# Kernel tuning notes

Measured on AMD Instinct MI355X. Metric: run time of the kernel, lower is better.

## Reference

```python
import jax, jax.numpy as jnp
import numpy as np
import math

N, E, D, H, C, ED = 50000, 400000, 128, 8, 16, 64
HC = H * C  # == D (required by residual)
EPS = 1e-5


def _gelu(x):
    return 0.5 * x * (1.0 + jax.lax.erf(x / math.sqrt(2.0)))


def _layer_norm(x, g, b):
    m = jnp.mean(x, axis=-1, keepdims=True)
    v = jnp.mean(jnp.square(x - m), axis=-1, keepdims=True)
    return (x - m) * jax.lax.rsqrt(v + EPS) * g + b


def _batch_norm(x, g, b):
    # BatchNorm1d training-mode math: stats over the batch (row) dim
    m = jnp.mean(x, axis=0)
    v = jnp.mean(jnp.square(x - m), axis=0)
    return (x - m) * jax.lax.rsqrt(v + EPS) * g + b


def setup_inputs() -> dict:
    key = jax.random.key(0)
    ks = jax.random.split(key, 40)
    s = 0.05
    inp = {
        "x": jax.random.normal(ks[0], (N, D), jnp.float32),
        "edge_index": jax.random.randint(ks[1], (2, E), 0, N, jnp.int64),
        "edge_attr": jax.random.normal(ks[2], (E, ED), jnp.float32),
        # attention projections
        "Wq": jax.random.normal(ks[3], (D, HC), jnp.float32) * s,
        "bq": jnp.zeros((HC,), jnp.float32),
        "Wk": jax.random.normal(ks[4], (D, HC), jnp.float32) * s,
        "bk": jnp.zeros((HC,), jnp.float32),
        "Wv": jax.random.normal(ks[5], (D, HC), jnp.float32) * s,
        "bv": jnp.zeros((HC,), jnp.float32),
        "We": jax.random.normal(ks[6], (ED, HC), jnp.float32) * s,  # no bias
        "Wke": jax.random.normal(ks[7], (3 * C, C), jnp.float32) * s,
        "bke": jnp.zeros((C,), jnp.float32),
        "Wve": jax.random.normal(ks[8], (3 * C, C), jnp.float32) * s,
        "bve": jnp.zeros((C,), jnp.float32),
        "Wfce": jax.random.normal(ks[9], (HC, ED), jnp.float32) * s,
        "bfce": jnp.zeros((ED,), jnp.float32),
        "lne_g": jnp.ones((ED,), jnp.float32),
        "lne_b": jnp.zeros((ED,), jnp.float32),
        "Wfcn": jax.random.normal(ks[10], (HC, D), jnp.float32) * s,
        "bfcn": jnp.zeros((D,), jnp.float32),
        "lnn_g": jnp.ones((D,), jnp.float32),
        "lnn_b": jnp.zeros((D,), jnp.float32),
        # FFN
        "W1n": jax.random.normal(ks[11], (D, 4 * D), jnp.float32) * s,
        "b1n": jnp.zeros((4 * D,), jnp.float32),
        "W2n": jax.random.normal(ks[12], (4 * D, D), jnp.float32) * s,
        "b2n": jnp.zeros((D,), jnp.float32),
        "W1e": jax.random.normal(ks[13], (ED, 4 * ED), jnp.float32) * s,
        "b1e": jnp.zeros((4 * ED,), jnp.float32),
        "W2e": jax.random.normal(ks[14], (4 * ED, ED), jnp.float32) * s,
        "b2e": jnp.zeros((ED,), jnp.float32),
        "bnn_g": jnp.ones((D,), jnp.float32),
        "bnn_b": jnp.zeros((D,), jnp.float32),
        "bne_g": jnp.ones((ED,), jnp.float32),
        "bne_b": jnp.zeros((ED,), jnp.float32),
    }
    return inp


def _forward(x, edge_attr, Wq, bq, Wk, bk, Wv, bv, We, Wke, bke, Wve, bve,
             Wfce, bfce, lne_g, lne_b, Wfcn, bfcn, lnn_g, lnn_b,
             W1n, b1n, W2n, b2n, W1e, b1e, W2e, b2e,
             bnn_g, bnn_b, bne_g, bne_b, edge_index):
    src = edge_index[0]  # j (source)
    dst = edge_index[1]  # i (target / aggregation index)

    Q = (x @ Wq + bq).reshape(N, H, C)
    K = (x @ Wk + bk).reshape(N, H, C)
    V = (x @ Wv + bv).reshape(N, H, C)

    Qi = Q[dst]                                  # [E,H,C]
    e = (edge_attr @ We).reshape(E, H, C)        # W_e(edge_attr)

    # K_e(cat([K_i, K_j, e])) as three C x C matmuls (avoids big concat)
    Wk1, Wk2, Wk3 = Wke[:C], Wke[C:2 * C], Wke[2 * C:]
    Knew = (jnp.einsum('ehc,cd->ehd', K[dst], Wk1)
            + jnp.einsum('ehc,cd->ehd', K[src], Wk2)
            + jnp.einsum('ehc,cd->ehd', e, Wk3) + bke)

    logits = jnp.sum(Qi * Knew, axis=-1) / math.sqrt(C)   # [E,H]
    # segment softmax over target nodes (PyG softmax)
    mx = jax.ops.segment_max(logits, dst, num_segments=N)  # [N,H]
    ex = jnp.exp(logits - mx[dst])
    den = jax.ops.segment_sum(ex, dst, num_segments=N)
    alpha = ex / (den[dst] + 1e-16)                        # [E,H]

    Wv1, Wv2, Wv3 = Wve[:C], Wve[C:2 * C], Wve[2 * C:]
    Vnew = (jnp.einsum('ehc,cd->ehd', V[dst], Wv1)
            + jnp.einsum('ehc,cd->ehd', V[src], Wv2)
            + jnp.einsum('ehc,cd->ehd', e, Wv3) + bve)

    edge_store = e * alpha[..., None]                      # saved self.edge_attr
    msg = Vnew * alpha[..., None]
    out = jax.ops.segment_sum(msg, dst, num_segments=N)    # [N,H,C]

    e_out = _layer_norm(edge_store.reshape(E, HC) @ Wfce + bfce, lne_g, lne_b) + edge_attr
    x_out = _layer_norm(out.reshape(N, HC) @ Wfcn + bfcn, lnn_g, lnn_b) + x

    # PoswiseFeedForwardNetwork
    x2 = _batch_norm(_gelu(x_out @ W1n + b1n) @ W2n + b2n, bnn_g, bnn_b) + x_out
    e2 = _batch_norm(_gelu(e_out @ W1e + b1e) @ W2e + b2e, bne_g, bne_b) + e_out
    return jax.nn.softplus(x2), jax.nn.softplus(e2)


def reference(x, edge_index, edge_attr, Wq, bq, Wk, bk, Wv, bv, We, Wke, bke,
              Wve, bve, Wfce, bfce, lne_g, lne_b, Wfcn, bfcn, lnn_g, lnn_b,
              W1n, b1n, W2n, b2n, W1e, b1e, W2e, b2e, bnn_g, bnn_b, bne_g, bne_b):
    return _forward(x, edge_attr, Wq, bq, Wk, bk, Wv, bv, We, Wke, bke, Wve, bve,
                    Wfce, bfce, lne_g, lne_b, Wfcn, bfcn, lnn_g, lnn_b,
                    W1n, b1n, W2n, b2n, W1e, b1e, W2e, b2e,
                    bnn_g, bnn_b, bne_g, bne_b, edge_index)
```

## Files before the change

### kernel.cpp

```cpp
#include <hip/hip_runtime.h>
#include <math.h>
#include <stdint.h>

#define N_NODES 50000
#define E_EDGES 400000
#define DIM 128
#define HEADS 8
#define CH 16
#define EDIM 64
#define HCDIM 128

#define EPCHUNK 100000
#define NODE_WAVES 4

using bf16x8 = __attribute__((ext_vector_type(8))) short;
using f32x4v = __attribute__((ext_vector_type(4))) float;


__global__ void fill_kernel(float* p, float v, int n) {
    int i = blockIdx.x * blockDim.x + threadIdx.x;
    if (i < n) p[i] = v;
}

__global__ void concat3_kernel(const float* __restrict__ a, const float* __restrict__ b,
                               const float* __restrict__ c, float* __restrict__ o) {
    int i = blockIdx.x * 256 + threadIdx.x;
    if (i < 128) o[i] = a[i];
    else if (i < 256) o[i] = b[i - 128];
    else if (i < 384) o[i] = c[i - 256];
}

__device__ inline float gelu_f(float x) {
    return 0.5f * x * (1.0f + erff(x * 0.70710678118654752f));
}

__device__ inline float softplus_f(float x) {
    return x > 20.f ? x : log1pf(expf(x));
}

__device__ inline unsigned short f32_to_bf16_rn(float f) {
    unsigned u = __float_as_uint(f);
    u += 0x7FFFu + ((u >> 16) & 1u);
    return (unsigned short)(u >> 16);
}
__device__ inline float bf16_to_f32(unsigned short h) {
    return __uint_as_float((unsigned)h << 16);
}

__global__ __launch_bounds__(256) void wsplit_kernel(
    const float* __restrict__ W, unsigned short* __restrict__ hi,
    unsigned short* __restrict__ lo, int K, int N)
{
    int idx = blockIdx.x * 256 + threadIdx.x;
    if (idx >= K * N) return;
    int n = idx / K, k = idx - n * K;
    float x = W[(size_t)k * N + n];
    unsigned short h = f32_to_bf16_rn(x);
    hi[idx] = h;
    lo[idx] = f32_to_bf16_rn(x - bf16_to_f32(h));
}

template<int BN>
__global__ __launch_bounds__(256) void gemm_mfma(
    const float* __restrict__ A,
    const unsigned short* __restrict__ Whi, const unsigned short* __restrict__ Wlo,
    const float* __restrict__ bias, const float* __restrict__ ascale,
    float* __restrict__ C, int M, int K, int Nc, int act, int cmode)
{
    constexpr int MT = (BN == 128) ? 4 : 2;
    __shared__ bf16x8 As[2][4][128];

    const int tid = threadIdx.x;
    const int w = tid >> 6, lane = tid & 63;
    const int l15 = lane & 15, lg = lane >> 4;
    const int m0 = blockIdx.y * 128;
    const int n0 = blockIdx.x * BN;
    const int rowbase = (BN == 128) ? (w >> 1) * 64 : w * 32;
    const int colbase = (BN == 128) ? (w & 1) * 64 : 0;
    const int k16 = K >> 4;

    f32x4v acc[MT][4];
#pragma unroll
    for (int i = 0; i < MT; ++i)
#pragma unroll
        for (int j = 0; j < 4; ++j)
#pragma unroll
            for (int cidx = 0; cidx < 4; ++cidx) acc[i][j][cidx] = 0.f;

    for (int k0 = 0; k0 < K; k0 += 32) {
#pragma unroll
        for (int it = 0; it < 2; ++it) {
            int row = w * 16 + l15 + it * 64;
            int ar = m0 + row;
            float v[8];
            if (ar < M) {
                const float* ap = A + (size_t)ar * K + k0 + lg * 8;
                *(float4*)&v[0] = *(const float4*)ap;
                *(float4*)&v[4] = *(const float4*)(ap + 4);
                if (ascale) {
                    float s = ascale[(size_t)ar * k16 + ((k0 >> 4) + (lg >> 1))];
#pragma unroll
                    for (int j = 0; j < 8; ++j) v[j] *= s;
                }
            } else {
#pragma unroll
                for (int j = 0; j < 8; ++j) v[j] = 0.f;
            }
            bf16x8 gh, gl;
#pragma unroll
            for (int j = 0; j < 8; ++j) {
                unsigned short h = f32_to_bf16_rn(v[j]);
                gh[j] = (short)h;
                gl[j] = (short)f32_to_bf16_rn(v[j] - bf16_to_f32(h));
            }
            As[0][lg][row] = gh;
            As[1][lg][row] = gl;
        }
        bf16x8 bh[4], bl[4];
#pragma unroll
        for (int nt = 0; nt < 4; ++nt) {
            size_t off = (size_t)(n0 + colbase + nt * 16 + l15) * K + k0 + lg * 8;
            bh[nt] = *(const bf16x8*)(Whi + off);
            bl[nt] = *(const bf16x8*)(Wlo + off);
        }
        __syncthreads();
#pragma unroll
        for (int mt = 0; mt < MT; ++mt) {
            int arow = rowbase + mt * 16 + l15;
            bf16x8 ah = As[0][lg][arow];
            bf16x8 al = As[1][lg][arow];
#pragma unroll
            for (int nt = 0; nt < 4; ++nt) {
                acc[mt][nt] = __builtin_amdgcn_mfma_f32_16x16x32_bf16(ah, bh[nt], acc[mt][nt], 0, 0, 0);
                acc[mt][nt] = __builtin_amdgcn_mfma_f32_16x16x32_bf16(al, bh[nt], acc[mt][nt], 0, 0, 0);
                acc[mt][nt] = __builtin_amdgcn_mfma_f32_16x16x32_bf16(ah, bl[nt], acc[mt][nt], 0, 0, 0);
            }
        }
        __syncthreads();
    }

#pragma unroll
    for (int nt = 0; nt < 4; ++nt) {
        int col = n0 + colbase + nt * 16 + l15;
        float bb = bias ? bias[col] : 0.f;
#pragma unroll
        for (int mt = 0; mt < MT; ++mt) {
#pragma unroll
            for (int i = 0; i < 4; ++i) {
                int r = m0 + rowbase + mt * 16 + lg * 4 + i;
                if (r < M) {
                    float o = acc[mt][nt][i] + bb;
                    if (act == 1) o = gelu_f(o);
                    if (cmode == 1) {
                        C[(size_t)(col >> 7) * ((size_t)N_NODES * HCDIM) + (size_t)r * HCDIM + (col & 127)] = o;
                    } else {
                        C[(size_t)r * Nc + col] = o;
                    }
                }
            }
        }
    }
}

static inline void launch_mfma(const float* A, const unsigned short* Whi, const unsigned short* Wlo,
                               const float* bias, const float* ascale, float* C,
                               int M, int K, int Nc, int act, int cmode, hipStream_t stream)
{
    int gy = (M + 127) / 128;
    if (Nc % 128 == 0)
        gemm_mfma<128><<<dim3(Nc / 128, gy), dim3(256), 0, stream>>>(A, Whi, Wlo, bias, ascale, C, M, K, Nc, act, cmode);
    else
        gemm_mfma<64><<<dim3(Nc / 64, gy), dim3(256), 0, stream>>>(A, Whi, Wlo, bias, ascale, C, M, K, Nc, act, cmode);
}

template<int BM, int K1, int NH, int N2, int ACT1, int ASC, int LN2>
__global__ __launch_bounds__(256) void ffn2_fused(
    const float* __restrict__ A,
    const unsigned short* __restrict__ W1hi, const unsigned short* __restrict__ W1lo,
    const float* __restrict__ b1,
    const unsigned short* __restrict__ W2hi, const unsigned short* __restrict__ W2lo,
    const float* __restrict__ b2,
    const float* __restrict__ ascale,
    const float* __restrict__ lng, const float* __restrict__ lnb,
    const float* __restrict__ resid,
    float* __restrict__ Cout, int M)
{
    constexpr int MT = BM / 64;
    constexpr int NT2 = N2 / 16;
    constexpr int NK = K1 / 32;
    __shared__ unsigned short Hs[2][BM][64];

    const int tid = threadIdx.x;
    const int w = tid >> 6, lane = tid & 63;
    const int l15 = lane & 15, lg = lane >> 4;
    const int m0 = blockIdx.x * BM;
    const int wr0 = w * (BM / 4);

    bf16x8 aA[2][MT][NK];
#pragma unroll
    for (int mt = 0; mt < MT; ++mt) {
        int ar = m0 + wr0 + mt * 16 + l15;
#pragma unroll
        for (int t = 0; t < NK; ++t) {
            float v[8];
            if (ar < M) {
                const float* ap = A + (size_t)ar * K1 + t * 32 + lg * 8;
                *(float4*)&v[0] = *(const float4*)ap;
                *(float4*)&v[4] = *(const float4*)(ap + 4);
            } else {
#pragma unroll
                for (int j = 0; j < 8; ++j) v[j] = 0.f;
            }
            bf16x8 gh, gl;
#pragma unroll
            for (int j = 0; j < 8; ++j) {
                unsigned short h = f32_to_bf16_rn(v[j]);
                gh[j] = (short)h;
                gl[j] = (short)f32_to_bf16_rn(v[j] - bf16_to_f32(h));
            }
            aA[0][mt][t] = gh;
            aA[1][mt][t] = gl;
        }
    }

    f32x4v oacc[MT][NT2];
#pragma unroll
    for (int mt = 0; mt < MT; ++mt)
#pragma unroll
        for (int nt = 0; nt < NT2; ++nt)
#pragma unroll
            for (int cidx = 0; cidx < 4; ++cidx) oacc[mt][nt][cidx] = 0.f;

    for (int hc = 0; hc < NH; hc += 64) {
        f32x4v acc1[MT][4];
#pragma unroll
        for (int mt = 0; mt < MT; ++mt)
#pragma unroll
            for (int nt = 0; nt < 4; ++nt)
#pragma unroll
                for (int cidx = 0; cidx < 4; ++cidx) acc1[mt][nt][cidx] = 0.f;

#pragma unroll
        for (int t = 0; t < NK; ++t) {
            bf16x8 bh[4], bl[4];
#pragma unroll
            for (int nt = 0; nt < 4; ++nt) {
                size_t off = (size_t)(hc + nt * 16 + l15) * K1 + t * 32 + lg * 8;
                bh[nt] = *(const bf16x8*)(W1hi + off);
                bl[nt] = *(const bf16x8*)(W1lo + off);
            }
#pragma unroll
            for (int mt = 0; mt < MT; ++mt) {
                bf16x8 ah = aA[0][mt][t];
                bf16x8 al = aA[1][mt][t];
#pragma unroll
                for (int nt = 0; nt < 4; ++nt) {
                    acc1[mt][nt] = __builtin_amdgcn_mfma_f32_16x16x32_bf16(ah, bh[nt], acc1[mt][nt], 0, 0, 0);
                    acc1[mt][nt] = __builtin_amdgcn_mfma_f32_16x16x32_bf16(al, bh[nt], acc1[mt][nt], 0, 0, 0);
                    acc1[mt][nt] = __builtin_amdgcn_mfma_f32_16x16x32_bf16(ah, bl[nt], acc1[mt][nt], 0, 0, 0);
                }
            }
        }

        __syncthreads();
#pragma unroll
        for (int nt = 0; nt < 4; ++nt) {
            float b1v = b1 ? b1[hc + nt * 16 + l15] : 0.f;
#pragma unroll
            for (int mt = 0; mt < MT; ++mt) {
#pragma unroll
                for (int i = 0; i < 4; ++i) {
                    int row = wr0 + mt * 16 + lg * 4 + i;
                    float o = acc1[mt][nt][i] + b1v;
                    if (ACT1) o = gelu_f(o);
                    if (ASC) {
                        int r = m0 + row;
                        float s = (r < M) ? ascale[(size_t)r * (NH >> 4) + (hc >> 4) + nt] : 0.f;
                        o *= s;
                    }
                    unsigned short hh = f32_to_bf16_rn(o);
                    unsigned short hl = f32_to_bf16_rn(o - bf16_to_f32(hh));
                    int slot = (nt * 16 + l15) ^ ((row & 7) << 3);
                    Hs[0][row][slot] = hh;
                    Hs[1][row][slot] = hl;
                }
            }
        }
        __syncthreads();

#pragma unroll
        for (int k2 = 0; k2 < 64; k2 += 32) {
            bf16x8 b2h[NT2], b2l[NT2];
#pragma unroll
            for (int nt = 0; nt < NT2; ++nt) {
                size_t off = (size_t)(nt * 16 + l15) * NH + hc + k2 + lg * 8;
                b2h[nt] = *(const bf16x8*)(W2hi + off);
                b2l[nt] = *(const bf16x8*)(W2lo + off);
            }
#pragma unroll
            for (int mt = 0; mt < MT; ++mt) {
                int row = wr0 + mt * 16 + l15;
                int slot = (k2 + lg * 8) ^ ((row & 7) << 3);
                bf16x8 ah = *(const bf16x8*)&Hs[0][row][slot];
                bf16x8 al = *(const bf16x8*)&Hs[1][row][slot];
#pragma unroll
                for (int nt = 0; nt < NT2; ++nt) {
                    oacc[mt][nt] = __builtin_amdgcn_mfma_f32_16x16x32_bf16(ah, b2h[nt], oacc[mt][nt], 0, 0, 0);
                    oacc[mt][nt] = __builtin_amdgcn_mfma_f32_16x16x32_bf16(al, b2h[nt], oacc[mt][nt], 0, 0, 0);
                    oacc[mt][nt] = __builtin_amdgcn_mfma_f32_16x16x32_bf16(ah, b2l[nt], oacc[mt][nt], 0, 0, 0);
                }
            }
        }
    }

    if (LN2) {
        float b2v[4], gv[4], bv[4];
#pragma unroll
        for (int nt = 0; nt < NT2; ++nt) {
            int col = nt * 16 + l15;
            b2v[nt] = b2 ? b2[col] : 0.f;
            gv[nt] = lng[col];
            bv[nt] = lnb[col];
        }
#pragma unroll
        for (int mt = 0; mt < MT; ++mt) {
#pragma unroll
            for (int i = 0; i < 4; ++i) {
                int r = m0 + wr0 + mt * 16 + lg * 4 + i;
                float o[4];
                float s = 0.f;
#pragma unroll
                for (int nt = 0; nt < NT2; ++nt) { o[nt] = oacc[mt][nt][i] + b2v[nt]; s += o[nt]; }
                s += __shfl_xor(s, 1); s += __shfl_xor(s, 2); s += __shfl_xor(s, 4); s += __shfl_xor(s, 8);
                float mean = s * (1.f / 64.f);
                float q = 0.f;
                float d[4];
#pragma unroll
                for (int nt = 0; nt < NT2; ++nt) { d[nt] = o[nt] - mean; q += d[nt] * d[nt]; }
                q += __shfl_xor(q, 1); q += __shfl_xor(q, 2); q += __shfl_xor(q, 4); q += __shfl_xor(q, 8);
                float inv = rsqrtf(q * (1.f / 64.f) + 1e-5f);
                if (r < M) {
#pragma unroll
                    for (int nt = 0; nt < NT2; ++nt) {
                        int col = nt * 16 + l15;
                        Cout[(size_t)r * N2 + col] = d[nt] * inv * gv[nt] + bv[nt] + resid[(size_t)r * N2 + col];
                    }
                }
            }
        }
    } else {
#pragma unroll
        for (int nt = 0; nt < NT2; ++nt) {
            int col = nt * 16 + l15;
            float bb = b2 ? b2[col] : 0.f;
#pragma unroll
            for (int mt = 0; mt < MT; ++mt) {
#pragma unroll
                for (int i = 0; i < 4; ++i) {
                    int r = m0 + wr0 + mt * 16 + lg * 4 + i;
                    if (r < M) Cout[(size_t)r * N2 + col] = oacc[mt][nt][i] + bb;
                }
            }
        }
    }
}

__global__ __launch_bounds__(256) void wex_kernel(
    const float* __restrict__ We, const float* __restrict__ X, float* __restrict__ out)
{
    int idx = blockIdx.x * 256 + threadIdx.x;
    if (idx >= 64 * 128) return;
    int k = idx >> 7, hj = idx & 127, h = hj >> 4, j = hj & 15;
    float s = 0.f;
#pragma unroll
    for (int c = 0; c < 16; ++c) s += We[k * 128 + h * 16 + c] * X[c * 16 + j];
    out[idx] = s;
}

__global__ __launch_bounds__(256) void qk_pre_kernel(
    const float* __restrict__ Q, const float* __restrict__ K,
    const float* __restrict__ Wke, const float* __restrict__ bke,
    float* __restrict__ A2, float* __restrict__ c0)
{
    __shared__ float wk1[256], wk2[256], bks[16];
    for (int i = threadIdx.x; i < 256; i += 256) { wk1[i] = Wke[i]; wk2[i] = Wke[256 + i]; }
    if (threadIdx.x < 16) bks[threadIdx.x] = bke[threadIdx.x];
    __syncthreads();
    int idx = blockIdx.x * 256 + threadIdx.x;
    int j = idx & 15; int dh = idx >> 4; int h = dh & 7; int d = dh >> 3;
    if (d >= N_NODES) return;
    const float* q = Q + (size_t)d * HCDIM + h * CH;
    const float* k = K + (size_t)d * HCDIM + h * CH;
    float qv[16], kv[16];
#pragma unroll
    for (int t = 0; t < 4; ++t) {
        *(float4*)&qv[t * 4] = *(const float4*)(q + t * 4);
        *(float4*)&kv[t * 4] = *(const float4*)(k + t * 4);
    }
    float a2 = 0.f;
#pragma unroll
    for (int t = 0; t < 16; ++t) a2 += wk2[j * 16 + t] * qv[t];
    A2[idx] = a2;
    float kn = bks[j];
#pragma unroll
    for (int c = 0; c < 16; ++c) kn += kv[c] * wk1[c * 16 + j];
    float t = qv[j] * kn;
    t += __shfl_xor(t, 1); t += __shfl_xor(t, 2); t += __shfl_xor(t, 4); t += __shfl_xor(t, 8);
    if (j == 0) c0[dh] = t;
}

__global__ __launch_bounds__(256) void logits_kernel(
    const float* __restrict__ Q, const float* __restrict__ K,
    const float* __restrict__ A2, const float* __restrict__ c0,
    const float* __restrict__ ep3,
    const int* __restrict__ src, const int* __restrict__ dst,
    float* __restrict__ logits, int e0, int ecnt)
{
    int idx = blockIdx.x * 256 + threadIdx.x;
    if (idx >= ecnt * HEADS) return;
    int el = idx >> 3, h = idx & 7, e = e0 + el;
    int s = src[e], d = dst[e];
    const float* q  = Q  + (size_t)d * HCDIM + h * CH;
    const float* a2 = A2 + (size_t)d * HCDIM + h * CH;
    const float* ks = K  + (size_t)s * HCDIM + h * CH;
    const float* ep = ep3 + (size_t)el * HCDIM + h * CH;
    float acc = c0[(size_t)d * HEADS + h];
    float qv[16], av[16], kv[16], ev[16];
#pragma unroll
    for (int t = 0; t < 4; ++t) {
        *(float4*)&qv[t * 4] = *(const float4*)(q + t * 4);
        *(float4*)&av[t * 4] = *(const float4*)(a2 + t * 4);
        *(float4*)&kv[t * 4] = *(const float4*)(ks + t * 4);
        *(float4*)&ev[t * 4] = *(const float4*)(ep + t * 4);
    }
#pragma unroll
    for (int t = 0; t < 16; ++t) acc += av[t] * kv[t] + qv[t] * ev[t];
    logits[(size_t)e * HEADS + h] = acc * 0.25f;
}

__global__ __launch_bounds__(256) void count_kernel(const int* __restrict__ dst, int* __restrict__ cnt) {
    int e = blockIdx.x * 256 + threadIdx.x;
    if (e < E_EDGES) atomicAdd(&cnt[dst[e]], 1);
}

__global__ __launch_bounds__(1024) void scan_kernel(
    const int* __restrict__ cnt, int* __restrict__ rowptr, int* __restrict__ cursor, int n)
{
    __shared__ int buf[1024];
    __shared__ int base;
    int tid = threadIdx.x;
    if (tid == 0) { base = 0; rowptr[0] = 0; }
    __syncthreads();
    for (int t0 = 0; t0 < n; t0 += 1024) {
        int i = t0 + tid;
        int v = (i < n) ? cnt[i] : 0;
        buf[tid] = v;
        __syncthreads();
        for (int off = 1; off < 1024; off <<= 1) {
            int add = (tid >= off) ? buf[tid - off] : 0;
            __syncthreads();
            buf[tid] += add;
            __syncthreads();
        }
        if (i < n) { rowptr[i + 1] = base + buf[tid]; cursor[i] = base + buf[tid] - v; }
        __syncthreads();
        if (tid == 0) base += buf[1023];
        __syncthreads();
    }
}

__global__ __launch_bounds__(256) void scatter_kernel(
    const int* __restrict__ dst, int* __restrict__ cursor, int* __restrict__ eidx) {
    int e = blockIdx.x * 256 + threadIdx.x;
    if (e < E_EDGES) {
        int p = atomicAdd(&cursor[dst[e]], 1);
        eidx[p] = e;
    }
}

__global__ __launch_bounds__(256) void node_attn_kernel(
    const float* __restrict__ Vb, const float* __restrict__ edge_attr,
    float* __restrict__ logits,
    const int* __restrict__ rowptr, const int* __restrict__ eidx,
    const int* __restrict__ src,
    const float* __restrict__ Wve, const float* __restrict__ bve,
    const float* __restrict__ WeWv3, float* __restrict__ aggout)
{
    __shared__ float wv1s[256], wv2s[256], bvs[16];
    __shared__ float stage[NODE_WAVES][640];

    for (int i = threadIdx.x; i < 256; i += 256) { wv1s[i] = Wve[i]; wv2s[i] = Wve[256 + i]; }
    if (threadIdx.x < 16) bvs[threadIdx.x] = bve[threadIdx.x];
    __syncthreads();

    int w = threadIdx.x >> 6, lane = threadIdx.x & 63;
    int d = blockIdx.x * NODE_WAVES + w;
    int r0 = rowptr[d], r1 = rowptr[d + 1], deg = r1 - r0;
    int h = lane >> 3, kg = lane & 7;

    if (deg == 0) {
        aggout[(size_t)d * HCDIM + lane] = 0.f;
        aggout[(size_t)d * HCDIM + 64 + lane] = 0.f;
    } else {
        float m[8], ssum[8];
#pragma unroll
        for (int t = 0; t < 8; ++t) { m[t] = -INFINITY; ssum[t] = 0.f; }
        for (int i = r0 + lane; i < r1; i += 64) {
            int e = eidx[i];
            const float* lp = logits + (size_t)e * HEADS;
            float l[8];
            *(float4*)&l[0] = *(const float4*)lp;
            *(float4*)&l[4] = *(const float4*)(lp + 4);
#pragma unroll
            for (int t = 0; t < 8; ++t) m[t] = fmaxf(m[t], l[t]);
        }
#pragma unroll
        for (int o = 1; o < 64; o <<= 1) {
#pragma unroll
            for (int t = 0; t < 8; ++t) m[t] = fmaxf(m[t], __shfl_xor(m[t], o));
        }
        for (int i = r0 + lane; i < r1; i += 64) {
            int e = eidx[i];
            const float* lp = logits + (size_t)e * HEADS;
            float l[8];
            *(float4*)&l[0] = *(const float4*)lp;
            *(float4*)&l[4] = *(const float4*)(lp + 4);
#pragma unroll
            for (int t = 0; t < 8; ++t) ssum[t] += expf(l[t] - m[t]);
        }
#pragma unroll
        for (int o = 1; o < 64; o <<= 1) {
#pragma unroll
            for (int t = 0; t < 8; ++t) ssum[t] += __shfl_xor(ssum[t], o);
        }
        float mh = m[0], dd = ssum[0];
#pragma unroll
        for (int t = 1; t < 8; ++t) { if (h == t) { mh = m[t]; dd = ssum[t]; } }
        float den = dd + 1e-16f;

        float wea[8] = {0.f, 0.f, 0.f, 0.f, 0.f, 0.f, 0.f, 0.f};
        float av0 = 0.f, av1 = 0.f;
        for (int i = r0; i < r1; ++i) {
            int e = eidx[i];
            float lg = logits[(size_t)e * HEADS + h];
            float alpha = expf(lg - mh) / den;
            if (kg == 0) logits[(size_t)e * HEADS + h] = alpha;
            int s = src[e];
            const float* ea = edge_attr + (size_t)e * EDIM + kg * 8;
            float ev[8];
            *(float4*)&ev[0] = *(const float4*)ea;
            *(float4*)&ev[4] = *(const float4*)(ea + 4);
#pragma unroll
            for (int t = 0; t < 8; ++t) wea[t] += alpha * ev[t];
            float2 vv = *(const float2*)(Vb + (size_t)s * HCDIM + h * CH + kg * 2);
            av0 += alpha * vv.x;
            av1 += alpha * vv.y;
        }
        float* st = stage[w];
#pragma unroll
        for (int t = 0; t < 8; ++t) st[h * 64 + kg * 8 + t] = wea[t];
        st[512 + h * 16 + kg * 2] = av0;
        st[512 + h * 16 + kg * 2 + 1] = av1;
    }
    __syncthreads();
    if (deg > 0) {
        float* st = stage[w];
        int c0i = kg * 2;
        float acc0 = bvs[c0i], acc1 = bvs[c0i + 1];
        const float* vd = Vb + (size_t)d * HCDIM + h * CH;
#pragma unroll
        for (int j = 0; j < 16; ++j) {
            float vj = vd[j];
            float a = st[512 + h * 16 + j];
            acc0 += vj * wv1s[j * 16 + c0i] + a * wv2s[j * 16 + c0i];
            acc1 += vj * wv1s[j * 16 + c0i + 1] + a * wv2s[j * 16 + c0i + 1];
        }
        const float* w3 = WeWv3 + h * 16 + c0i;
#pragma unroll 16
        for (int k = 0; k < 64; ++k) {
            float wv = st[h * 64 + k];
            float2 w2v = *(const float2*)(w3 + k * 128);
            acc0 += wv * w2v.x;
            acc1 += wv * w2v.y;
        }
        aggout[(size_t)d * HCDIM + h * CH + c0i] = acc0;
        aggout[(size_t)d * HCDIM + h * CH + c0i + 1] = acc1;
    }
}

__global__ __launch_bounds__(256) void ln_res_kernel(
    float* __restrict__ y, const float* __restrict__ g, const float* __restrict__ b,
    const float* __restrict__ res, int rows, int w)
{
    int wave = threadIdx.x >> 6;
    int lane = threadIdx.x & 63;
    int nw = blockDim.x >> 6;
    for (int r = blockIdx.x * nw + wave; r < rows; r += gridDim.x * nw) {
        size_t base = (size_t)r * w;
        float v0 = y[base + lane];
        float v1 = (w == 128) ? y[base + 64 + lane] : 0.f;
        float s = v0 + v1;
#pragma unroll
        for (int o = 32; o; o >>= 1) s += __shfl_xor(s, o);
        float m = s / (float)w;
        float d0 = v0 - m;
        float d1 = (w == 128) ? (v1 - m) : 0.f;
        float q = d0 * d0 + d1 * d1;
#pragma unroll
        for (int o = 32; o; o >>= 1) q += __shfl_xor(q, o);
        float inv = rsqrtf(q / (float)w + 1e-5f);
        y[base + lane] = d0 * inv * g[lane] + b[lane] + res[base + lane];
        if (w == 128)
            y[base + 64 + lane] = d1 * inv * g[64 + lane] + b[64 + lane] + res[base + 64 + lane];
    }
}

__global__ __launch_bounds__(256) void bn_stats_kernel(
    const float* __restrict__ y, float* __restrict__ colsum, float* __restrict__ colsq,
    int rows, int cols)
{
    __shared__ float ss[256], sq[256];
    int tid = threadIdx.x;
    int col = tid % cols;
    int rsub = tid / cols;
    int rstep = blockDim.x / cols;
    float ls = 0.f, lq = 0.f;
    for (int r = blockIdx.x * rstep + rsub; r < rows; r += gridDim.x * rstep) {
        float v = y[(size_t)r * cols + col];
        ls += v;
        lq += v * v;
    }
    ss[tid] = ls;
    sq[tid] = lq;
    __syncthreads();
    if (tid < cols) {
        for (int o = cols; o < 256; o += cols) { ls += ss[tid + o]; lq += sq[tid + o]; }
        atomicAdd(&colsum[tid], ls);
        atomicAdd(&colsq[tid], lq);
    }
}

__global__ __launch_bounds__(256) void bn_apply_softplus_kernel(
    const float* __restrict__ y, const float* __restrict__ res,
    const float* __restrict__ colsum, const float* __restrict__ colsq,
    const float* __restrict__ g, const float* __restrict__ b,
    float* __restrict__ out, int rows, int cols)
{
    int idx = blockIdx.x * blockDim.x + threadIdx.x;
    int n = rows * cols;
    if (idx >= n) return;
    int c = idx % cols;
    float m = colsum[c] / (float)rows;
    float var = colsq[c] / (float)rows - m * m;
    float inv = rsqrtf(var + 1e-5f);
    float v = (y[idx] - m) * inv * g[c] + b[c] + res[idx];
    out[idx] = softplus_f(v);
}


extern "C" void kernel_launch(void* const* d_in, const int* in_sizes, int n_in,
                              void* d_out, int out_size, void* d_ws, size_t ws_size,
                              hipStream_t stream) {
    const float* x         = (const float*)d_in[0];
    const int*   ei        = (const int*)d_in[1];
    const float* edge_attr = (const float*)d_in[2];
    const float* Wq  = (const float*)d_in[3];
    const float* bq  = (const float*)d_in[4];
    const float* Wk  = (const float*)d_in[5];
    const float* bk  = (const float*)d_in[6];
    const float* Wv  = (const float*)d_in[7];
    const float* bv  = (const float*)d_in[8];
    const float* We  = (const float*)d_in[9];
    const float* Wke = (const float*)d_in[10];
    const float* bke = (const float*)d_in[11];
    const float* Wve = (const float*)d_in[12];
    const float* bve = (const float*)d_in[13];
    const float* Wfce = (const float*)d_in[14];
    const float* bfce = (const float*)d_in[15];
    const float* lne_g = (const float*)d_in[16];
    const float* lne_b = (const float*)d_in[17];
    const float* Wfcn = (const float*)d_in[18];
    const float* bfcn = (const float*)d_in[19];
    const float* lnn_g = (const float*)d_in[20];
    const float* lnn_b = (const float*)d_in[21];
    const float* W1n = (const float*)d_in[22];
    const float* b1n = (const float*)d_in[23];
    const float* W2n = (const float*)d_in[24];
    const float* b2n = (const float*)d_in[25];
    const float* W1e = (const float*)d_in[26];
    const float* b1e = (const float*)d_in[27];
    const float* W2e = (const float*)d_in[28];
    const float* b2e = (const float*)d_in[29];
    const float* bnn_g = (const float*)d_in[30];
    const float* bnn_b = (const float*)d_in[31];
    const float* bne_g = (const float*)d_in[32];
    const float* bne_b = (const float*)d_in[33];

    const int* src = ei;
    const int* dst = ei + E_EDGES;

    float* ws = (float*)d_ws;
    const size_t M64   = (size_t)E_EDGES * EDIM;
    const size_t NODE2 = (size_t)N_NODES * HCDIM;

    float* regionR = ws;
    float* Qb  = regionR;
    float* Kb  = regionR + NODE2;
    float* Vb  = regionR + 2 * NODE2;

    float* overlayY = ws + M64;
    float* logits = overlayY;
    float* c0buf  = logits + (size_t)E_EDGES * HEADS;
    int*   cnt_i    = (int*)(c0buf + (size_t)N_NODES * HEADS);
    int*   rowptr_i = cnt_i + N_NODES;
    int*   cursor_i = rowptr_i + N_NODES + 1;
    int*   eidx_i   = cursor_i + N_NODES;
    float* aggout = (float*)(((uintptr_t)(eidx_i + E_EDGES) + 15) & ~(uintptr_t)15);
    float* y_n    = aggout + NODE2;
    float* x_out  = y_n + NODE2;
    float* y_e    = overlayY;
    float* epbig  = y_n;

    float* e_out = ws + 2 * M64;
    float* A2buf = e_out;

    float* tail = ws + 3 * M64;
    float* colsum_n = tail;
    float* colsq_n  = tail + 128;
    float* colsum_e = tail + 256;
    float* colsq_e  = tail + 320;
    float* WeK3  = tail + 384;
    float* WeWv3 = WeK3 + 8192;
    float* bqkv  = WeWv3 + 8192;

    unsigned short* wsp = (unsigned short*)(bqkv + 384);
    unsigned short* QKV_s  = wsp;
    unsigned short* WeK3_s = QKV_s  + 2 * 49152;
    unsigned short* We_s   = WeK3_s + 2 * 8192;
    unsigned short* Wfce_s = We_s   + 2 * 8192;
    unsigned short* Wfcn_s = Wfce_s + 2 * 8192;
    unsigned short* W1n_s  = Wfcn_s + 2 * 16384;
    unsigned short* W2n_s  = W1n_s  + 2 * 65536;
    unsigned short* W1e_s  = W2n_s  + 2 * 65536;
    unsigned short* W2e_s  = W1e_s  + 2 * 16384;

    dim3 blk(256);

    fill_kernel<<<dim3(2), blk, 0, stream>>>(colsum_n, 0.f, 384);
    fill_kernel<<<dim3((N_NODES + 255) / 256), blk, 0, stream>>>((float*)cnt_i, 0.f, N_NODES);

    wex_kernel<<<dim3(32), blk, 0, stream>>>(We, Wke + 2 * CH * CH, WeK3);
    wex_kernel<<<dim3(32), blk, 0, stream>>>(We, Wve + 2 * CH * CH, WeWv3);

    wsplit_kernel<<<dim3(64), blk, 0, stream>>>(Wq, QKV_s,          QKV_s + 49152,          128, 128);
    wsplit_kernel<<<dim3(64), blk, 0, stream>>>(Wk, QKV_s + 16384,  QKV_s + 49152 + 16384,  128, 128);
    wsplit_kernel<<<dim3(64), blk, 0, stream>>>(Wv, QKV_s + 32768,  QKV_s + 49152 + 32768,  128, 128);
    wsplit_kernel<<<dim3(32), blk, 0, stream>>>(WeK3, WeK3_s, WeK3_s + 8192,  64, 128);
    wsplit_kernel<<<dim3(32), blk, 0, stream>>>(We,   We_s,   We_s + 8192,    64, 128);
    wsplit_kernel<<<dim3(32), blk, 0, stream>>>(Wfce, Wfce_s, Wfce_s + 8192,  128, 64);
    wsplit_kernel<<<dim3(64), blk, 0, stream>>>(Wfcn, Wfcn_s, Wfcn_s + 16384, 128, 128);
    wsplit_kernel<<<dim3(256), blk, 0, stream>>>(W1n, W1n_s, W1n_s + 65536,   128, 512);
    wsplit_kernel<<<dim3(256), blk, 0, stream>>>(W2n, W2n_s, W2n_s + 65536,   512, 128);
    wsplit_kernel<<<dim3(64), blk, 0, stream>>>(W1e, W1e_s, W1e_s + 16384,    64, 256);
    wsplit_kernel<<<dim3(64), blk, 0, stream>>>(W2e, W2e_s, W2e_s + 16384,    256, 64);
    concat3_kernel<<<dim3(2), blk, 0, stream>>>(bq, bk, bv, bqkv);

    launch_mfma(x, QKV_s, QKV_s + 49152, bqkv, nullptr, Qb, N_NODES, 128, 384, 0, 1, stream);

    qk_pre_kernel<<<dim3(N_NODES * HCDIM / 256), blk, 0, stream>>>(Qb, Kb, Wke, bke, A2buf, c0buf);

    count_kernel<<<dim3((E_EDGES + 255) / 256), blk, 0, stream>>>(dst, cnt_i);
    scan_kernel<<<dim3(1), dim3(1024), 0, stream>>>(cnt_i, rowptr_i, cursor_i, N_NODES);
    scatter_kernel<<<dim3((E_EDGES + 255) / 256), blk, 0, stream>>>(dst, cursor_i, eidx_i);

    for (int e0 = 0; e0 < E_EDGES; e0 += EPCHUNK) {
        launch_mfma(edge_attr + (size_t)e0 * EDIM, WeK3_s, WeK3_s + 8192, nullptr, nullptr,
                    epbig, EPCHUNK, EDIM, HCDIM, 0, 0, stream);
        logits_kernel<<<dim3((EPCHUNK * HEADS + 255) / 256), blk, 0, stream>>>(
            Qb, Kb, A2buf, c0buf, epbig, src, dst, logits, e0, EPCHUNK);
    }

    node_attn_kernel<<<dim3(N_NODES / NODE_WAVES), blk, 0, stream>>>(
        Vb, edge_attr, logits, rowptr_i, eidx_i, src, Wve, bve, WeWv3, aggout);

    ffn2_fused<128, 64, 128, 64, 0, 1, 1><<<dim3(E_EDGES / 128), blk, 0, stream>>>(
        edge_attr, We_s, We_s + 8192, nullptr, Wfce_s, Wfce_s + 8192, bfce,
        logits, lne_g, lne_b, edge_attr, e_out, E_EDGES);

    launch_mfma(aggout, Wfcn_s, Wfcn_s + 16384, bfcn, nullptr, x_out, N_NODES, HCDIM, DIM, 0, 0, stream);
    ln_res_kernel<<<dim3(12500), blk, 0, stream>>>(x_out, lnn_g, lnn_b, x, N_NODES, DIM);

    ffn2_fused<64, 128, 512, 128, 1, 0, 0><<<dim3((N_NODES + 63) / 64), blk, 0, stream>>>(
        x_out, W1n_s, W1n_s + 65536, b1n, W2n_s, W2n_s + 65536, b2n,
        nullptr, nullptr, nullptr, nullptr, y_n, N_NODES);
    bn_stats_kernel<<<dim3(256), blk, 0, stream>>>(y_n, colsum_n, colsq_n, N_NODES, DIM);
    {
        int n = N_NODES * DIM;
        bn_apply_softplus_kernel<<<dim3((n + 255) / 256), blk, 0, stream>>>(
            y_n, x_out, colsum_n, colsq_n, bnn_g, bnn_b, (float*)d_out, N_NODES, DIM);
    }

    ffn2_fused<128, 64, 256, 64, 1, 0, 0><<<dim3(E_EDGES / 128), blk, 0, stream>>>(
        e_out, W1e_s, W1e_s + 16384, b1e, W2e_s, W2e_s + 16384, b2e,
        nullptr, nullptr, nullptr, nullptr, y_e, E_EDGES);
    bn_stats_kernel<<<dim3(256), blk, 0, stream>>>(y_e, colsum_e, colsq_e, E_EDGES, EDIM);
    {
        int n = E_EDGES * EDIM;
        bn_apply_softplus_kernel<<<dim3((n + 255) / 256), blk, 0, stream>>>(
            y_e, e_out, colsum_e, colsq_e, bne_g, bne_b, (float*)d_out + (size_t)N_NODES * DIM, E_EDGES, EDIM);
    }
}
```

Baseline: 2.182 ms.

## Keep fused FFN hidden activations in registers, removing LDS staging and barriers

Rewrites the fused two-layer FFN kernel so each wave computes the transposed first-layer product (weights as A operand, activations as B). The MFMA output layout then directly forms the bf16 B-operand fragment for the second GEMM, with no shared memory or __syncthreads. To match that register layout, the second-layer weights are pre-split with a permuted K order. This removes LDS traffic and block-level synchronisation and makes output stores float4-vectorised, but it reloads weights per wave and relies on the K permutation being exactly correct.

```diff
diff --git a/kernel.cpp b/kernel.cpp
--- a/kernel.cpp
+++ b/kernel.cpp
@@ -55,6 +55,22 @@
     if (idx >= K * N) return;
     int n = idx / K, k = idx - n * K;
     float x = W[(size_t)k * N + n];
+    unsigned short h = f32_to_bf16_rn(x);
+    hi[idx] = h;
+    lo[idx] = f32_to_bf16_rn(x - bf16_to_f32(h));
+}
+
+__global__ __launch_bounds__(256) void wsplit_perm_kernel(
+    const float* __restrict__ W, unsigned short* __restrict__ hi,
+    unsigned short* __restrict__ lo, int K, int N)
+{
+    int idx = blockIdx.x * 256 + threadIdx.x;
+    if (idx >= K * N) return;
+    int n = idx / K, k = idx - n * K;
+    int s = k & 31, base = k & ~31;
+    int lgp = s >> 3, j = s & 7;
+    int ksrc = base + ((j < 4) ? (lgp * 4 + j) : (16 + lgp * 4 + (j - 4)));
+    float x = W[(size_t)ksrc * N + n];
     unsigned short h = f32_to_bf16_rn(x);
     hi[idx] = h;
     lo[idx] = f32_to_bf16_rn(x - bf16_to_f32(h));
@@ -173,8 +189,8 @@
         gemm_mfma<64><<<dim3(Nc / 64, gy), dim3(256), 0, stream>>>(A, Whi, Wlo, bias, ascale, C, M, K, Nc, act, cmode);
 }
 
-template<int BM, int K1, int NH, int N2, int ACT1, int ASC, int LN2>
-__global__ __launch_bounds__(256) void ffn2_fused(
+template<int MT, int K1, int NH, int N2, int ACT1, int ASC, int LN2>
+__global__ __launch_bounds__(256) void ffn2_nobar(
     const float* __restrict__ A,
     const unsigned short* __restrict__ W1hi, const unsigned short* __restrict__ W1lo,
     const float* __restrict__ b1,
@@ -185,26 +201,24 @@
     const float* __restrict__ resid,
     float* __restrict__ Cout, int M)
 {
-    constexpr int MT = BM / 64;
+    constexpr int NK = K1 / 32;
     constexpr int NT2 = N2 / 16;
-    constexpr int NK = K1 / 32;
-    __shared__ unsigned short Hs[2][BM][64];
-
+    constexpr int NI = NH / 16;
+    constexpr int NP = NH / 32;
     const int tid = threadIdx.x;
     const int w = tid >> 6, lane = tid & 63;
     const int l15 = lane & 15, lg = lane >> 4;
-    const int m0 = blockIdx.x * BM;
-    const int wr0 = w * (BM / 4);
-
-    bf16x8 aA[2][MT][NK];
+    const int row0 = (blockIdx.x * 4 + w) * (MT * 16);
+
+    bf16x8 aAh[MT][NK], aAl[MT][NK];
 #pragma unroll
     for (int mt = 0; mt < MT; ++mt) {
-        int ar = m0 + wr0 + mt * 16 + l15;
-#pragma unroll
-        for (int t = 0; t < NK; ++t) {
+        int r = row0 + mt * 16 + l15;
+#pragma unroll
+        for (int ks = 0; ks < NK; ++ks) {
             float v[8];
-            if (ar < M) {
-                const float* ap = A + (size_t)ar * K1 + t * 32 + lg * 8;
+            if (r < M) {
+                const float* ap = A + (size_t)r * K1 + ks * 32 + lg * 8;
                 *(float4*)&v[0] = *(const float4*)ap;
                 *(float4*)&v[4] = *(const float4*)(ap + 4);
             } else {
@@ -218,8 +232,8 @@
                 gh[j] = (short)h;
                 gl[j] = (short)f32_to_bf16_rn(v[j] - bf16_to_f32(h));
             }
-            aA[0][mt][t] = gh;
-            aA[1][mt][t] = gl;
+            aAh[mt][ks] = gh;
+            aAl[mt][ks] = gl;
         }
     }
 
@@ -229,136 +243,121 @@
 #pragma unroll
         for (int nt = 0; nt < NT2; ++nt)
 #pragma unroll
-            for (int cidx = 0; cidx < 4; ++cidx) oacc[mt][nt][cidx] = 0.f;
-
-    for (int hc = 0; hc < NH; hc += 64) {
-        f32x4v acc1[MT][4];
-#pragma unroll
-        for (int mt = 0; mt < MT; ++mt)
-#pragma unroll
-            for (int nt = 0; nt < 4; ++nt)
-#pragma unroll
-                for (int cidx = 0; cidx < 4; ++cidx) acc1[mt][nt][cidx] = 0.f;
-
-#pragma unroll
-        for (int t = 0; t < NK; ++t) {
-            bf16x8 bh[4], bl[4];
-#pragma unroll
-            for (int nt = 0; nt < 4; ++nt) {
-                size_t off = (size_t)(hc + nt * 16 + l15) * K1 + t * 32 + lg * 8;
-                bh[nt] = *(const bf16x8*)(W1hi + off);
-                bl[nt] = *(const bf16x8*)(W1lo + off);
-            }
+            for (int c = 0; c < 4; ++c) oacc[mt][nt][c] = 0.f;
+
+    for (int p = 0; p < NP; ++p) {
+        bf16x8 hh[MT], hl[MT];
+#pragma unroll
+        for (int half = 0; half < 2; ++half) {
+            const int it = p * 2 + half;
+            f32x4v h[MT];
+#pragma unroll
+            for (int mt = 0; mt < MT; ++mt)
+#pragma unroll
+                for (int c = 0; c < 4; ++c) h[mt][c] = 0.f;
+#pragma unroll
+            for (int ks = 0; ks < NK; ++ks) {
+                size_t off = (size_t)(it * 16 + l15) * K1 + ks * 32 + lg * 8;
+                bf16x8 xh = *(const bf16x8*)(W1hi + off);
+                bf16x8 xl = *(const bf16x8*)(W1lo + off);
+#pragma unroll
+                for (int mt = 0; mt < MT; ++mt) {
+                    h[mt] = __builtin_amdgcn_mfma_f32_16x16x32_bf16(xh, aAh[mt][ks], h[mt], 0, 0, 0);
+                    h[mt] = __builtin_amdgcn_mfma_f32_16x16x32_bf16(xl, aAh[mt][ks], h[mt], 0, 0, 0);
+                    h[mt] = __builtin_amdgcn_mfma_f32_16x16x32_bf16(xh, aAl[mt][ks], h[mt], 0, 0, 0);
+                }
+            }
+            float b1a[4] = {0.f, 0.f, 0.f, 0.f};
+            if (b1) *(float4*)b1a = *(const float4*)(b1 + it * 16 + lg * 4);
 #pragma unroll
             for (int mt = 0; mt < MT; ++mt) {
-                bf16x8 ah = aA[0][mt][t];
-                bf16x8 al = aA[1][mt][t];
-#pragma unroll
-                for (int nt = 0; nt < 4; ++nt) {
-                    acc1[mt][nt] = __builtin_amdgcn_mfma_f32_16x16x32_bf16(ah, bh[nt], acc1[mt][nt], 0, 0, 0);
-                    acc1[mt][nt] = __builtin_amdgcn_mfma_f32_16x16x32_bf16(al, bh[nt], acc1[mt][nt], 0, 0, 0);
-                    acc1[mt][nt] = __builtin_amdgcn_mfma_f32_16x16x32_bf16(ah, bl[nt], acc1[mt][nt], 0, 0, 0);
+                float sc = 1.f;
+                if (ASC) {
+                    int r = row0 + mt * 16 + l15;
+                    sc = (r < M) ? ascale[(size_t)r * NI + it] : 0.f;
                 }
-            }
-        }
-
-        __syncthreads();
-#pragma unroll
-        for (int nt = 0; nt < 4; ++nt) {
-            float b1v = b1 ? b1[hc + nt * 16 + l15] : 0.f;
+#pragma unroll
+                for (int i = 0; i < 4; ++i) {
+                    float o = h[mt][i] + b1a[i];
+                    if (ACT1) o = gelu_f(o);
+                    if (ASC) o *= sc;
+                    unsigned short oh = f32_to_bf16_rn(o);
+                    hh[mt][half * 4 + i] = (short)oh;
+                    hl[mt][half * 4 + i] = (short)f32_to_bf16_rn(o - bf16_to_f32(oh));
+                }
+            }
+        }
+#pragma unroll
+        for (int nt2 = 0; nt2 < NT2; ++nt2) {
+            size_t off2 = (size_t)(nt2 * 16 + l15) * NH + p * 32 + lg * 8;
+            bf16x8 x2h = *(const bf16x8*)(W2hi + off2);
+            bf16x8 x2l = *(const bf16x8*)(W2lo + off2);
 #pragma unroll
             for (int mt = 0; mt < MT; ++mt) {
-#pragma unroll
-                for (int i = 0; i < 4; ++i) {
-                    int row = wr0 + mt * 16 + lg * 4 + i;
-                    float o = acc1[mt][nt][i] + b1v;
-                    if (ACT1) o = gelu_f(o);
-                    if (ASC) {
-                        int r = m0 + row;
-                        float s = (r < M) ? ascale[(size_t)r * (NH >> 4) + (hc >> 4) + nt] : 0.f;
-                        o *= s;
-                    }
-                    unsigned short hh = f32_to_bf16_rn(o);
-                    unsigned short hl = f32_to_bf16_rn(o - bf16_to_f32(hh));
-                    int slot = (nt * 16 + l15) ^ ((row & 7) << 3);
-                    Hs[0][row][slot] = hh;
-                    Hs[1][row][slot] = hl;
+                oacc[mt][nt2] = __builtin_amdgcn_mfma_f32_16x16x32_bf16(x2h, hh[mt], oacc[mt][nt2], 0, 0, 0);
+                oacc[mt][nt2] = __builtin_amdgcn_mfma_f32_16x16x32_bf16(x2l, hh[mt], oacc[mt][nt2], 0, 0, 0);
+                oacc[mt][nt2] = __builtin_amdgcn_mfma_f32_16x16x32_bf16(x2h, hl[mt], oacc[mt][nt2], 0, 0, 0);
+            }
+        }
+    }
+
+    float b2a[NT2][4];
+#pragma unroll
+    for (int nt2 = 0; nt2 < NT2; ++nt2) {
+        if (b2) *(float4*)b2a[nt2] = *(const float4*)(b2 + nt2 * 16 + lg * 4);
+        else { b2a[nt2][0] = 0.f; b2a[nt2][1] = 0.f; b2a[nt2][2] = 0.f; b2a[nt2][3] = 0.f; }
+    }
+    if (LN2) {
+        float ga[NT2][4], bba[NT2][4];
+#pragma unroll
+        for (int nt2 = 0; nt2 < NT2; ++nt2) {
+            *(float4*)ga[nt2] = *(const float4*)(lng + nt2 * 16 + lg * 4);
+            *(float4*)bba[nt2] = *(const float4*)(lnb + nt2 * 16 + lg * 4);
+        }
+#pragma unroll
+        for (int mt = 0; mt < MT; ++mt) {
+            int r = row0 + mt * 16 + l15;
+            float o[NT2][4];
+            float s = 0.f;
+#pragma unroll
+            for (int nt2 = 0; nt2 < NT2; ++nt2)
+#pragma unroll
+                for (int i = 0; i < 4; ++i) { o[nt2][i] = oacc[mt][nt2][i] + b2a[nt2][i]; s += o[nt2][i]; }
+            s += __shfl_xor(s, 16); s += __shfl_xor(s, 32);
+            float mean = s * (1.f / (float)N2);
+            float q = 0.f;
+#pragma unroll
+            for (int nt2 = 0; nt2 < NT2; ++nt2)
+#pragma unroll
+                for (int i = 0; i < 4; ++i) { o[nt2][i] -= mean; q += o[nt2][i] * o[nt2][i]; }
+            q += __shfl_xor(q, 16); q += __shfl_xor(q, 32);
+            float inv = rsqrtf(q * (1.f / (float)N2) + 1e-5f);
+            if (r < M) {
+#pragma unroll
+                for (int nt2 = 0; nt2 < NT2; ++nt2) {
+                    float4 rv = *(const float4*)(resid + (size_t)r * N2 + nt2 * 16 + lg * 4);
+                    float4 ov;
+                    ov.x = o[nt2][0] * inv * ga[nt2][0] + bba[nt2][0] + rv.x;
+                    ov.y = o[nt2][1] * inv * ga[nt2][1] + bba[nt2][1] + rv.y;
+                    ov.z = o[nt2][2] * inv * ga[nt2][2] + bba[nt2][2] + rv.z;
+                    ov.w = o[nt2][3] * inv * ga[nt2][3] + bba[nt2][3] + rv.w;
+                    *(float4*)(Cout + (size_t)r * N2 + nt2 * 16 + lg * 4) = ov;
                 }
             }
         }
-        __syncthreads();
-
-#pragma unroll
-        for (int k2 = 0; k2 < 64; k2 += 32) {
-            bf16x8 b2h[NT2], b2l[NT2];
-#pragma unroll
-            for (int nt = 0; nt < NT2; ++nt) {
-                size_t off = (size_t)(nt * 16 + l15) * NH + hc + k2 + lg * 8;
-                b2h[nt] = *(const bf16x8*)(W2hi + off);
-                b2l[nt] = *(const bf16x8*)(W2lo + off);
-            }
-#pragma unroll
-            for (int mt = 0; mt < MT; ++mt) {
-                int row = wr0 + mt * 16 + l15;
-                int slot = (k2 + lg * 8) ^ ((row & 7) << 3);
-                bf16x8 ah = *(const bf16x8*)&Hs[0][row][slot];
-                bf16x8 al = *(const bf16x8*)&Hs[1][row][slot];
-#pragma unroll
-                for (int nt = 0; nt < NT2; ++nt) {
-                    oacc[mt][nt] = __builtin_amdgcn_mfma_f32_16x16x32_bf16(ah, b2h[nt], oacc[mt][nt], 0, 0, 0);
-                    oacc[mt][nt] = __builtin_amdgcn_mfma_f32_16x16x32_bf16(al, b2h[nt], oacc[mt][nt], 0, 0, 0);
-                    oacc[mt][nt] = __builtin_amdgcn_mfma_f32_16x16x32_bf16(ah, b2l[nt], oacc[mt][nt], 0, 0, 0);
-                }
-            }
-        }
-    }
-
-    if (LN2) {
-        float b2v[4], gv[4], bv[4];
-#pragma unroll
-        for (int nt = 0; nt < NT2; ++nt) {
-            int col = nt * 16 + l15;
-            b2v[nt] = b2 ? b2[col] : 0.f;
-            gv[nt] = lng[col];
-            bv[nt] = lnb[col];
-        }
+    } else {
 #pragma unroll
         for (int mt = 0; mt < MT; ++mt) {
-#pragma unroll
-            for (int i = 0; i < 4; ++i) {
-                int r = m0 + wr0 + mt * 16 + lg * 4 + i;
-                float o[4];
-                float s = 0.f;
-#pragma unroll
-                for (int nt = 0; nt < NT2; ++nt) { o[nt] = oacc[mt][nt][i] + b2v[nt]; s += o[nt]; }
-                s += __shfl_xor(s, 1); s += __shfl_xor(s, 2); s += __shfl_xor(s, 4); s += __shfl_xor(s, 8);
-                float mean = s * (1.f / 64.f);
-                float q = 0.f;
-                float d[4];
-#pragma unroll
-                for (int nt = 0; nt < NT2; ++nt) { d[nt] = o[nt] - mean; q += d[nt] * d[nt]; }
-                q += __shfl_xor(q, 1); q += __shfl_xor(q, 2); q += __shfl_xor(q, 4); q += __shfl_xor(q, 8);
-                float inv = rsqrtf(q * (1.f / 64.f) + 1e-5f);
-                if (r < M) {
-#pragma unroll
-                    for (int nt = 0; nt < NT2; ++nt) {
-                        int col = nt * 16 + l15;
-                        Cout[(size_t)r * N2 + col] = d[nt] * inv * gv[nt] + bv[nt] + resid[(size_t)r * N2 + col];
-                    }
-                }
-            }
-        }
-    } else {
-#pragma unroll
-        for (int nt = 0; nt < NT2; ++nt) {
-            int col = nt * 16 + l15;
-            float bb = b2 ? b2[col] : 0.f;
-#pragma unroll
-            for (int mt = 0; mt < MT; ++mt) {
-#pragma unroll
-                for (int i = 0; i < 4; ++i) {
-                    int r = m0 + wr0 + mt * 16 + lg * 4 + i;
-                    if (r < M) Cout[(size_t)r * N2 + col] = oacc[mt][nt][i] + bb;
+            int r = row0 + mt * 16 + l15;
+            if (r < M) {
+#pragma unroll
+                for (int nt2 = 0; nt2 < NT2; ++nt2) {
+                    float4 ov;
+                    ov.x = oacc[mt][nt2][0] + b2a[nt2][0];
+                    ov.y = oacc[mt][nt2][1] + b2a[nt2][1];
+                    ov.z = oacc[mt][nt2][2] + b2a[nt2][2];
+                    ov.w = oacc[mt][nt2][3] + b2a[nt2][3];
+                    *(float4*)(Cout + (size_t)r * N2 + nt2 * 16 + lg * 4) = ov;
                 }
             }
         }
@@ -757,12 +756,12 @@
     wsplit_kernel<<<dim3(64), blk, 0, stream>>>(Wv, QKV_s + 32768,  QKV_s + 49152 + 32768,  128, 128);
     wsplit_kernel<<<dim3(32), blk, 0, stream>>>(WeK3, WeK3_s, WeK3_s + 8192,  64, 128);
     wsplit_kernel<<<dim3(32), blk, 0, stream>>>(We,   We_s,   We_s + 8192,    64, 128);
-    wsplit_kernel<<<dim3(32), blk, 0, stream>>>(Wfce, Wfce_s, Wfce_s + 8192,  128, 64);
+    wsplit_perm_kernel<<<dim3(32), blk, 0, stream>>>(Wfce, Wfce_s, Wfce_s + 8192,  128, 64);
     wsplit_kernel<<<dim3(64), blk, 0, stream>>>(Wfcn, Wfcn_s, Wfcn_s + 16384, 128, 128);
     wsplit_kernel<<<dim3(256), blk, 0, stream>>>(W1n, W1n_s, W1n_s + 65536,   128, 512);
-    wsplit_kernel<<<dim3(256), blk, 0, stream>>>(W2n, W2n_s, W2n_s + 65536,   512, 128);
+    wsplit_perm_kernel<<<dim3(256), blk, 0, stream>>>(W2n, W2n_s, W2n_s + 65536,   512, 128);
     wsplit_kernel<<<dim3(64), blk, 0, stream>>>(W1e, W1e_s, W1e_s + 16384,    64, 256);
-    wsplit_kernel<<<dim3(64), blk, 0, stream>>>(W2e, W2e_s, W2e_s + 16384,    256, 64);
+    wsplit_perm_kernel<<<dim3(64), blk, 0, stream>>>(W2e, W2e_s, W2e_s + 16384,    256, 64);
     concat3_kernel<<<dim3(2), blk, 0, stream>>>(bq, bk, bv, bqkv);
 
     launch_mfma(x, QKV_s, QKV_s + 49152, bqkv, nullptr, Qb, N_NODES, 128, 384, 0, 1, stream);
@@ -783,14 +782,14 @@
     node_attn_kernel<<<dim3(N_NODES / NODE_WAVES), blk, 0, stream>>>(
         Vb, edge_attr, logits, rowptr_i, eidx_i, src, Wve, bve, WeWv3, aggout);
 
-    ffn2_fused<128, 64, 128, 64, 0, 1, 1><<<dim3(E_EDGES / 128), blk, 0, stream>>>(
+    ffn2_nobar<2, 64, 128, 64, 0, 1, 1><<<dim3(E_EDGES / 128), blk, 0, stream>>>(
         edge_attr, We_s, We_s + 8192, nullptr, Wfce_s, Wfce_s + 8192, bfce,
         logits, lne_g, lne_b, edge_attr, e_out, E_EDGES);
 
     launch_mfma(aggout, Wfcn_s, Wfcn_s + 16384, bfcn, nullptr, x_out, N_NODES, HCDIM, DIM, 0, 0, stream);
     ln_res_kernel<<<dim3(12500), blk, 0, stream>>>(x_out, lnn_g, lnn_b, x, N_NODES, DIM);
 
-    ffn2_fused<64, 128, 512, 128, 1, 0, 0><<<dim3((N_NODES + 63) / 64), blk, 0, stream>>>(
+    ffn2_nobar<1, 128, 512, 128, 1, 0, 0><<<dim3((N_NODES + 63) / 64), blk, 0, stream>>>(
         x_out, W1n_s, W1n_s + 65536, b1n, W2n_s, W2n_s + 65536, b2n,
         nullptr, nullptr, nullptr, nullptr, y_n, N_NODES);
     bn_stats_kernel<<<dim3(256), blk, 0, stream>>>(y_n, colsum_n, colsq_n, N_NODES, DIM);
@@ -800,7 +799,7 @@
             y_n, x_out, colsum_n, colsq_n, bnn_g, bnn_b, (float*)d_out, N_NODES, DIM);
     }
 
-    ffn2_fused<128, 64, 256, 64, 1, 0, 0><<<dim3(E_EDGES / 128), blk, 0, stream>>>(
+    ffn2_nobar<2, 64, 256, 64, 1, 0, 0><<<dim3(E_EDGES / 128), blk, 0, stream>>>(
         e_out, W1e_s, W1e_s + 16384, b1e, W2e_s, W2e_s + 16384, b2e,
         nullptr, nullptr, nullptr, nullptr, y_e, E_EDGES);
     bn_stats_kernel<<<dim3(256), blk, 0, stream>>>(y_e, colsum_e, colsq_e, E_EDGES, EDIM);
```

New measurement: 2.043 ms. 1.07x faster.
